# Optimization experiments

Measured on AMD Instinct MI355X. Metric: run time of the kernel, lower is better.

## Reference

```python
import jax, jax.numpy as jnp
import numpy as np

K = 0.001  # sigmoid temperature from DGCLoss init
EPS = 1e-8


def _off_diag(m):
    # [..., n, n] -> [..., n, n-1], removing the diagonal in row-major order
    n = m.shape[-1]
    lead = m.shape[:-2]
    flat = m.reshape(lead + (n * n,))[..., :-1]
    return flat.reshape(lead + (n - 1, n + 1))[..., 1:].reshape(lead + (n, n - 1))


def setup_inputs() -> dict:
    key = jax.random.key(0)
    k1, k2 = jax.random.split(key)
    ranking = jax.random.normal(k1, (384, 256), dtype=jnp.float32)
    gt = jax.random.randint(k2, (384,), 0, 6, dtype=jnp.int64)
    return {"ranking": ranking, "gt": gt}


def reference(ranking, gt):
    x = ranking
    N = x.shape[0]
    # cosine similarity matrix, mapped to [0, 1]
    xn = x / jnp.clip(jnp.linalg.norm(x, axis=1, keepdims=True), EPS, None)
    sm = (xn @ xn.T + 1.0) * 0.5                         # [N, N]
    rank = _off_diag(sm)                                 # [N, N-1]
    g = jnp.abs(gt[None, :] - gt[:, None]).astype(jnp.float32)  # [N, N]
    g = _off_diag(g)                                     # [N, N-1]
    M = N - 1
    # dij[n, i, j] = rank[n, j] - rank[n, i]
    dij = rank[:, None, :] - rank[:, :, None]            # [N, M, M]
    dij = _off_diag(dij)                                 # [N, M, M-1]
    # clamped sigmoid indicator
    indicator = 1.0 / (1.0 + jnp.exp(jnp.clip(-dij / K, -50.0, 50.0)))
    indicator = indicator.sum(-1) + 1.0                  # [N, M]
    relevance = jnp.exp2(jnp.clip(10.0 - g, 0.0, None)) - 1.0  # [N, M]
    dcg = (relevance / jnp.log2(indicator + 1.0)).sum(axis=1)  # [N]
    # ideal DCG from sorted relevance
    rel_sorted = jnp.sort(relevance, axis=-1)[:, ::-1]
    discount = jnp.log2(jnp.arange(M, dtype=jnp.float32) + 2.0)
    idcg = (rel_sorted / discount).sum(axis=-1)          # [N]
    valid = idcg != 0.0
    ndcg = jnp.where(valid, dcg / jnp.where(valid, idcg, 1.0), 0.0)
    cnt = valid.sum()
    mean_ndcg = ndcg.sum() / jnp.maximum(cnt, 1).astype(jnp.float32)
    return jnp.where(cnt == 0, jnp.float32(1.0), 1.0 - mean_ndcg)
```

## Files before the change

kernel.cpp:

```cpp
#include <hip/hip_runtime.h>


#define NN 384
#define DD 256
#define MM 383
#define HSCALE 721.3475204444817f
#define NBUCK  256
#define BSCALE 0.1767955801104972f
#define WWIN   12.0f

__global__ __launch_bounds__(256) void dgc_normT(const float* __restrict__ x,
                                                 float* __restrict__ XT,
                                                 float* __restrict__ XN) {
    __shared__ float xs[16][260];
    __shared__ float invn[16];

    const int t  = threadIdx.x;
    const int r0 = blockIdx.x * 16;

    #pragma unroll
    for (int i = 0; i < 4; ++i) {
        int f = t + i * 256;
        int r = f >> 6, c4 = f & 63;
        float4 v = ((const float4*)(x + (size_t)(r0 + r) * DD))[c4];
        xs[r][c4 * 4 + 0] = v.x; xs[r][c4 * 4 + 1] = v.y;
        xs[r][c4 * 4 + 2] = v.z; xs[r][c4 * 4 + 3] = v.w;
    }
    __syncthreads();

    {
        const int r = t >> 4, sub = t & 15;
        float s = 0.0f;
        #pragma unroll
        for (int m = 0; m < 16; ++m) {
            float v = xs[r][sub * 16 + m];
            s = fmaf(v, v, s);
        }
        #pragma unroll
        for (int off = 8; off > 0; off >>= 1) s += __shfl_xor(s, off, 64);
        if (sub == 0) invn[r] = __builtin_amdgcn_rsqf(fmaxf(s, 1e-16f));
    }
    __syncthreads();

    {
        const int r  = t & 15;
        const int kk = t >> 4;
        const float inv = invn[r];
        #pragma unroll
        for (int i = 0; i < 16; ++i) {
            int k = i * 16 + kk;
            XT[(size_t)k * NN + r0 + r] = xs[r][k] * inv;
        }
    }
    {
        #pragma unroll
        for (int i = 0; i < 4; ++i) {
            int f = t + i * 256;
            int r = f >> 6, c4 = f & 63;
            const float inv = invn[r];
            float4 v;
            v.x = xs[r][c4 * 4 + 0] * inv; v.y = xs[r][c4 * 4 + 1] * inv;
            v.z = xs[r][c4 * 4 + 2] * inv; v.w = xs[r][c4 * 4 + 3] * inv;
            ((float4*)(XN + (size_t)(r0 + r) * DD))[c4] = v;
        }
    }
}

__global__ __launch_bounds__(384) void dgc_fused(const float* __restrict__ XT,
                                                 const float* __restrict__ XN,
                                                 const int* __restrict__ gt,
                                                 float* __restrict__ ndcg) {
    __shared__ float  xs[DD];
    __shared__ float4 pacc[4][96];
    __shared__ float  srow[NN];
    __shared__ float  vsort[NN];
    __shared__ int    sidx[NN];
    __shared__ int    hist[NBUCK];
    __shared__ int    pre[NBUCK + 1];
    __shared__ int    wcnt[6][6];
    __shared__ int    gcum[6];
    __shared__ float  redd[6], redi[6];

    const int n    = blockIdx.x;
    const int t    = threadIdx.x;
    const int lane = t & 63;
    const int wave = t >> 6;

    if (t < DD / 4) ((float4*)xs)[t] = ((const float4*)(XN + (size_t)n * DD))[t];
    if (t < NBUCK) hist[t] = 0;
    __syncthreads();

    {
        const int j4 = t % 96;
        const int kc = t / 96;
        const float4* XT4 = (const float4*)XT;
        float4 a = {0.0f, 0.0f, 0.0f, 0.0f};
        const int k0 = kc * 64;
        #pragma unroll 8
        for (int m = 0; m < 64; ++m) {
            const int k = k0 + m;
            float4 b = XT4[(size_t)k * 96 + j4];
            float  s = xs[k];
            a.x = fmaf(s, b.x, a.x); a.y = fmaf(s, b.y, a.y);
            a.z = fmaf(s, b.z, a.z); a.w = fmaf(s, b.w, a.w);
        }
        pacc[kc][j4] = a;
    }
    __syncthreads();
    {
        const float* pf = (const float*)pacc;
        float dot = pf[t] + pf[384 + t] + pf[768 + t] + pf[1152 + t];
        srow[t] = fmaf(dot, HSCALE, HSCALE);
    }
    __syncthreads();

    const float vraw = srow[t];
    const float sn   = srow[n];

    int b = (int)(vraw * BSCALE);
    b = b < 0 ? 0 : (b > NBUCK - 1 ? NBUCK - 1 : b);
    const int slot = atomicAdd(&hist[b], 1);

    const bool validc = (t < MM);
    int gi = 0;
    if (validc) {
        const int gd = gt[t + (t >= n ? 1 : 0)] - gt[n];
        gi = gd < 0 ? -gd : gd;
    }
    #pragma unroll
    for (int g = 0; g < 6; ++g) {
        unsigned long long m = __ballot(validc && (gi == g));
        if (lane == g) wcnt[wave][g] = __popcll(m);
    }
    __syncthreads();

    if (wave == 0) {
        const int s0 = hist[lane * 4 + 0], s1 = hist[lane * 4 + 1];
        const int s2 = hist[lane * 4 + 2], s3 = hist[lane * 4 + 3];
        const int sum = s0 + s1 + s2 + s3;
        int inc = sum;
        #pragma unroll
        for (int off = 1; off < 64; off <<= 1) {
            int u = __shfl_up(inc, off, 64);
            if (lane >= off) inc += u;
        }
        const int base = inc - sum;
        pre[lane * 4 + 0] = base;
        pre[lane * 4 + 1] = base + s0;
        pre[lane * 4 + 2] = base + s0 + s1;
        pre[lane * 4 + 3] = base + s0 + s1 + s2;
        if (lane == 63) pre[NBUCK] = inc;
    }
    if (t == 0) {
        int s = 0;
        #pragma unroll
        for (int g = 0; g < 6; ++g) {
            s += wcnt[0][g] + wcnt[1][g] + wcnt[2][g]
               + wcnt[3][g] + wcnt[4][g] + wcnt[5][g];
            gcum[g] = s;
        }
    }
    __syncthreads();

    {
        const int pos = pre[b] + slot;
        vsort[pos] = vraw;
        sidx[pos]  = t;
    }
    __syncthreads();

    const float ri    = vsort[t];
    const int   iorig = sidx[t];

    int Blo = (int)((ri - WWIN) * BSCALE);
    int Bhi = (int)((ri + WWIN) * BSCALE);
    Blo = Blo < 0 ? 0 : (Blo > NBUCK - 1 ? NBUCK - 1 : Blo);
    Bhi = Bhi < 0 ? 0 : (Bhi > NBUCK - 1 ? NBUCK - 1 : Bhi);
    const int lo = pre[Blo];
    const int hi = pre[Bhi + 1];

    float p0 = 0.0f, p1 = 0.0f;
    int q = lo;
    for (; q + 2 <= hi; q += 2) {
        p0 += __builtin_amdgcn_rcpf(1.0f + __builtin_amdgcn_exp2f(ri - vsort[q]));
        p1 += __builtin_amdgcn_rcpf(1.0f + __builtin_amdgcn_exp2f(ri - vsort[q + 1]));
    }
    if (q < hi)
        p0 += __builtin_amdgcn_rcpf(1.0f + __builtin_amdgcn_exp2f(ri - vsort[q]));
    float sum_all = (float)(NN - hi) + p0 + p1;

    int bn = (int)(sn * BSCALE);
    bn = bn < 0 ? 0 : (bn > NBUCK - 1 ? NBUCK - 1 : bn);
    float cd = 0.0f;
    if (bn > Bhi)       cd = 1.0f;
    else if (bn >= Blo) cd = __builtin_amdgcn_rcpf(1.0f + __builtin_amdgcn_exp2f(ri - sn));
    const float ind = 0.5f + sum_all - cd;

    float idcg_i = 0.0f;
    if (validc) {
        const int p = t;
        const int g = (p >= gcum[0]) + (p >= gcum[1]) + (p >= gcum[2])
                    + (p >= gcum[3]) + (p >= gcum[4]);
        idcg_i = (float)((1 << (10 - g)) - 1) / __builtin_amdgcn_logf((float)(p + 2));
    }

    float dcg_i = 0.0f;
    if (iorig != n) {
        const int gd = gt[iorig] - gt[n];
        const int gg = gd < 0 ? -gd : gd;
        dcg_i = (float)((1 << (10 - gg)) - 1) / __builtin_amdgcn_logf(ind + 1.0f);
    }

    #pragma unroll
    for (int off = 32; off > 0; off >>= 1) {
        dcg_i  += __shfl_down(dcg_i,  off, 64);
        idcg_i += __shfl_down(idcg_i, off, 64);
    }
    if (lane == 0) { redd[wave] = dcg_i; redi[wave] = idcg_i; }
    __syncthreads();
    if (t == 0) {
        float d = 0.0f, id = 0.0f;
        #pragma unroll
        for (int w = 0; w < 6; ++w) { d += redd[w]; id += redi[w]; }
        ndcg[n] = d / id;
    }
}

__global__ __launch_bounds__(384) void dgc_final(const float* __restrict__ ndcg,
                                                 float* __restrict__ out) {
    __shared__ float red[6];
    const int t    = threadIdx.x;
    const int lane = t & 63;
    const int wave = t >> 6;
    float nd = ndcg[t];
    #pragma unroll
    for (int off = 32; off > 0; off >>= 1) nd += __shfl_down(nd, off, 64);
    if (lane == 0) red[wave] = nd;
    __syncthreads();
    if (t == 0) {
        float s = 0.0f;
        for (int w = 0; w < 6; ++w) s += red[w];
        out[0] = 1.0f - s / (float)NN;
    }
}

extern "C" void kernel_launch(void* const* d_in, const int* in_sizes, int n_in,
                              void* d_out, int out_size, void* d_ws, size_t ws_size,
                              hipStream_t stream) {
    const float* ranking = (const float*)d_in[0];
    const int*   gt      = (const int*)d_in[1];
    float*       out     = (float*)d_out;

    float* XT   = (float*)d_ws;
    float* XN   = XT + (size_t)DD * NN;
    float* ndcg = XN + (size_t)NN * DD;

    dgc_normT<<<24, 256, 0, stream>>>(ranking, XT, XN);
    dgc_fused<<<NN, 384, 0, stream>>>(XT, XN, gt, ndcg);
    dgc_final<<<1, 384, 0, stream>>>(ndcg, out);
}
```

Measured before the change: 73.24 us.

## Process two rows per block, precompute IDCG table, narrow sigmoid window

The fused kernel now handles two query rows per 768-thread block, so each XT column load feeds two dot products and the matrix read traffic is halved. The ideal-DCG sum depends only on the query's gt class, so an extra block in the normalisation kernel computes it once into a six-entry table, which removes per-row ballot counting and a reduction. The sigmoid evaluation window shrinks from 12 to 6 scaled units, so fewer pairs are evaluated exactly. The narrower window adds approximation error for pairs whose sigmoid is not yet saturated, and the larger blocks use more shared memory, which may reduce occupancy.

After: 70.10 us. 1.04x faster.

```diff
diff --git a/kernel.cpp b/kernel.cpp
--- a/kernel.cpp
+++ b/kernel.cpp
@@ -7,15 +7,69 @@
 #define HSCALE 721.3475204444817f
 #define NBUCK  256
 #define BSCALE 0.1767955801104972f
-#define WWIN   12.0f
+#define WWIN   6.0f
 
 __global__ __launch_bounds__(256) void dgc_normT(const float* __restrict__ x,
+                                                 const int* __restrict__ gt,
                                                  float* __restrict__ XT,
-                                                 float* __restrict__ XN) {
+                                                 float* __restrict__ XN,
+                                                 float* __restrict__ idcg_tab) {
+    const int t = threadIdx.x;
+
+    if (blockIdx.x == 24) {
+        __shared__ int   cnt[6];
+        __shared__ int   cum[6][6];
+        __shared__ float wred[4][6];
+        const int lane = t & 63;
+        const int wave = t >> 6;
+
+        if (t < 6) cnt[t] = 0;
+        __syncthreads();
+        atomicAdd(&cnt[gt[t]], 1);
+        if (t + 256 < NN) atomicAdd(&cnt[gt[t + 256]], 1);
+        __syncthreads();
+        if (t < 6) {
+            int h[6];
+            #pragma unroll
+            for (int g = 0; g < 6; ++g) h[g] = 0;
+            #pragma unroll
+            for (int v = 0; v < 6; ++v) {
+                int d = v - t; d = d < 0 ? -d : d;
+                h[d] += cnt[v];
+            }
+            h[0] -= 1;
+            int s = 0;
+            #pragma unroll
+            for (int g = 0; g < 6; ++g) { s += h[g]; cum[t][g] = s; }
+        }
+        __syncthreads();
+
+        float acc[6] = {0.f, 0.f, 0.f, 0.f, 0.f, 0.f};
+        for (int p = t; p < MM; p += 256) {
+            const float invl = 1.0f / __builtin_amdgcn_logf((float)(p + 2));
+            #pragma unroll
+            for (int gv = 0; gv < 6; ++gv) {
+                const int g = (p >= cum[gv][0]) + (p >= cum[gv][1])
+                            + (p >= cum[gv][2]) + (p >= cum[gv][3])
+                            + (p >= cum[gv][4]);
+                acc[gv] += (float)((1 << (10 - g)) - 1) * invl;
+            }
+        }
+        for (int off = 32; off > 0; off >>= 1) {
+            #pragma unroll
+            for (int gv = 0; gv < 6; ++gv) acc[gv] += __shfl_down(acc[gv], off, 64);
+        }
+        if (lane == 0) {
+            #pragma unroll
+            for (int gv = 0; gv < 6; ++gv) wred[wave][gv] = acc[gv];
+        }
+        __syncthreads();
+        if (t < 6) idcg_tab[t] = wred[0][t] + wred[1][t] + wred[2][t] + wred[3][t];
+        return;
+    }
+
     __shared__ float xs[16][260];
     __shared__ float invn[16];
-
-    const int t  = threadIdx.x;
     const int r0 = blockIdx.x * 16;
 
     #pragma unroll
@@ -66,127 +120,119 @@
     }
 }
 
-__global__ __launch_bounds__(384) void dgc_fused(const float* __restrict__ XT,
+__global__ __launch_bounds__(768) void dgc_fused(const float* __restrict__ XT,
                                                  const float* __restrict__ XN,
                                                  const int* __restrict__ gt,
+                                                 const float* __restrict__ idcg_tab,
                                                  float* __restrict__ ndcg) {
-    __shared__ float  xs[DD];
-    __shared__ float4 pacc[4][96];
-    __shared__ float  srow[NN];
-    __shared__ float  vsort[NN];
-    __shared__ int    sidx[NN];
-    __shared__ int    hist[NBUCK];
-    __shared__ int    pre[NBUCK + 1];
-    __shared__ int    wcnt[6][6];
-    __shared__ int    gcum[6];
-    __shared__ float  redd[6], redi[6];
-
-    const int n    = blockIdx.x;
+    __shared__ float  xs[2][DD];
+    __shared__ float4 pacc[2][8][96];
+    __shared__ float  srow[2][NN];
+    __shared__ float  vsort[2][NN];
+    __shared__ int    sidx[2][NN];
+    __shared__ int    hist[2][NBUCK];
+    __shared__ int    pre[2][NBUCK + 1];
+    __shared__ float  redd[12];
+
+    const int n0   = blockIdx.x * 2;
     const int t    = threadIdx.x;
     const int lane = t & 63;
     const int wave = t >> 6;
 
-    if (t < DD / 4) ((float4*)xs)[t] = ((const float4*)(XN + (size_t)n * DD))[t];
-    if (t < NBUCK) hist[t] = 0;
+    if (t < 128)
+        ((float4*)xs[t >> 6])[t & 63] =
+            ((const float4*)(XN + (size_t)(n0 + (t >> 6)) * DD))[t & 63];
+    if (t < 512) ((int*)hist)[t] = 0;
     __syncthreads();
 
     {
         const int j4 = t % 96;
         const int kc = t / 96;
         const float4* XT4 = (const float4*)XT;
-        float4 a = {0.0f, 0.0f, 0.0f, 0.0f};
-        const int k0 = kc * 64;
+        float4 a0 = {0.f, 0.f, 0.f, 0.f};
+        float4 a1 = {0.f, 0.f, 0.f, 0.f};
+        const int k0 = kc * 32;
         #pragma unroll 8
-        for (int m = 0; m < 64; ++m) {
+        for (int m = 0; m < 32; ++m) {
             const int k = k0 + m;
             float4 b = XT4[(size_t)k * 96 + j4];
-            float  s = xs[k];
-            a.x = fmaf(s, b.x, a.x); a.y = fmaf(s, b.y, a.y);
-            a.z = fmaf(s, b.z, a.z); a.w = fmaf(s, b.w, a.w);
-        }
-        pacc[kc][j4] = a;
-    }
-    __syncthreads();
-    {
-        const float* pf = (const float*)pacc;
-        float dot = pf[t] + pf[384 + t] + pf[768 + t] + pf[1152 + t];
-        srow[t] = fmaf(dot, HSCALE, HSCALE);
-    }
-    __syncthreads();
-
-    const float vraw = srow[t];
-    const float sn   = srow[n];
-
+            float s0 = xs[0][k];
+            float s1 = xs[1][k];
+            a0.x = fmaf(s0, b.x, a0.x); a0.y = fmaf(s0, b.y, a0.y);
+            a0.z = fmaf(s0, b.z, a0.z); a0.w = fmaf(s0, b.w, a0.w);
+            a1.x = fmaf(s1, b.x, a1.x); a1.y = fmaf(s1, b.y, a1.y);
+            a1.z = fmaf(s1, b.z, a1.z); a1.w = fmaf(s1, b.w, a1.w);
+        }
+        pacc[0][kc][j4] = a0;
+        pacc[1][kc][j4] = a1;
+    }
+    __syncthreads();
+
+    const int r = t / 384;
+    const int u = t - r * 384;
+
+    {
+        const float* pf = (const float*)pacc[r];
+        float dot = 0.0f;
+        #pragma unroll
+        for (int c = 0; c < 8; ++c) dot += pf[c * 384 + u];
+        srow[r][u] = fmaf(dot, HSCALE, HSCALE);
+    }
+    __syncthreads();
+
+    const float vraw = srow[r][u];
     int b = (int)(vraw * BSCALE);
     b = b < 0 ? 0 : (b > NBUCK - 1 ? NBUCK - 1 : b);
-    const int slot = atomicAdd(&hist[b], 1);
-
-    const bool validc = (t < MM);
-    int gi = 0;
-    if (validc) {
-        const int gd = gt[t + (t >= n ? 1 : 0)] - gt[n];
-        gi = gd < 0 ? -gd : gd;
-    }
-    #pragma unroll
-    for (int g = 0; g < 6; ++g) {
-        unsigned long long m = __ballot(validc && (gi == g));
-        if (lane == g) wcnt[wave][g] = __popcll(m);
-    }
-    __syncthreads();
-
-    if (wave == 0) {
-        const int s0 = hist[lane * 4 + 0], s1 = hist[lane * 4 + 1];
-        const int s2 = hist[lane * 4 + 2], s3 = hist[lane * 4 + 3];
+    const int slot = atomicAdd(&hist[r][b], 1);
+    __syncthreads();
+
+    if (wave == 0 || wave == 6) {
+        const int rr = wave / 6;
+        const int s0 = hist[rr][lane * 4 + 0], s1 = hist[rr][lane * 4 + 1];
+        const int s2 = hist[rr][lane * 4 + 2], s3 = hist[rr][lane * 4 + 3];
         const int sum = s0 + s1 + s2 + s3;
         int inc = sum;
         #pragma unroll
         for (int off = 1; off < 64; off <<= 1) {
-            int u = __shfl_up(inc, off, 64);
-            if (lane >= off) inc += u;
+            int uu = __shfl_up(inc, off, 64);
+            if (lane >= off) inc += uu;
         }
         const int base = inc - sum;
-        pre[lane * 4 + 0] = base;
-        pre[lane * 4 + 1] = base + s0;
-        pre[lane * 4 + 2] = base + s0 + s1;
-        pre[lane * 4 + 3] = base + s0 + s1 + s2;
-        if (lane == 63) pre[NBUCK] = inc;
-    }
-    if (t == 0) {
-        int s = 0;
-        #pragma unroll
-        for (int g = 0; g < 6; ++g) {
-            s += wcnt[0][g] + wcnt[1][g] + wcnt[2][g]
-               + wcnt[3][g] + wcnt[4][g] + wcnt[5][g];
-            gcum[g] = s;
-        }
-    }
-    __syncthreads();
-
-    {
-        const int pos = pre[b] + slot;
-        vsort[pos] = vraw;
-        sidx[pos]  = t;
-    }
-    __syncthreads();
-
-    const float ri    = vsort[t];
-    const int   iorig = sidx[t];
+        pre[rr][lane * 4 + 0] = base;
+        pre[rr][lane * 4 + 1] = base + s0;
+        pre[rr][lane * 4 + 2] = base + s0 + s1;
+        pre[rr][lane * 4 + 3] = base + s0 + s1 + s2;
+        if (lane == 63) pre[rr][NBUCK] = inc;
+    }
+    __syncthreads();
+
+    {
+        const int pos = pre[r][b] + slot;
+        vsort[r][pos] = vraw;
+        sidx[r][pos]  = u;
+    }
+    __syncthreads();
+
+    const int   nrow  = n0 + r;
+    const float ri    = vsort[r][u];
+    const int   iorig = sidx[r][u];
+    const float sn    = srow[r][nrow];
 
     int Blo = (int)((ri - WWIN) * BSCALE);
     int Bhi = (int)((ri + WWIN) * BSCALE);
     Blo = Blo < 0 ? 0 : (Blo > NBUCK - 1 ? NBUCK - 1 : Blo);
     Bhi = Bhi < 0 ? 0 : (Bhi > NBUCK - 1 ? NBUCK - 1 : Bhi);
-    const int lo = pre[Blo];
-    const int hi = pre[Bhi + 1];
+    const int lo = pre[r][Blo];
+    const int hi = pre[r][Bhi + 1];
 
     float p0 = 0.0f, p1 = 0.0f;
     int q = lo;
     for (; q + 2 <= hi; q += 2) {
-        p0 += __builtin_amdgcn_rcpf(1.0f + __builtin_amdgcn_exp2f(ri - vsort[q]));
-        p1 += __builtin_amdgcn_rcpf(1.0f + __builtin_amdgcn_exp2f(ri - vsort[q + 1]));
+        p0 += __builtin_amdgcn_rcpf(1.0f + __builtin_amdgcn_exp2f(ri - vsort[r][q]));
+        p1 += __builtin_amdgcn_rcpf(1.0f + __builtin_amdgcn_exp2f(ri - vsort[r][q + 1]));
     }
     if (q < hi)
-        p0 += __builtin_amdgcn_rcpf(1.0f + __builtin_amdgcn_exp2f(ri - vsort[q]));
+        p0 += __builtin_amdgcn_rcpf(1.0f + __builtin_amdgcn_exp2f(ri - vsort[r][q]));
     float sum_all = (float)(NN - hi) + p0 + p1;
 
     int bn = (int)(sn * BSCALE);
@@ -196,34 +242,23 @@
     else if (bn >= Blo) cd = __builtin_amdgcn_rcpf(1.0f + __builtin_amdgcn_exp2f(ri - sn));
     const float ind = 0.5f + sum_all - cd;
 
-    float idcg_i = 0.0f;
-    if (validc) {
-        const int p = t;
-        const int g = (p >= gcum[0]) + (p >= gcum[1]) + (p >= gcum[2])
-                    + (p >= gcum[3]) + (p >= gcum[4]);
-        idcg_i = (float)((1 << (10 - g)) - 1) / __builtin_amdgcn_logf((float)(p + 2));
-    }
-
     float dcg_i = 0.0f;
-    if (iorig != n) {
-        const int gd = gt[iorig] - gt[n];
+    if (iorig != nrow) {
+        const int gd = gt[iorig] - gt[nrow];
         const int gg = gd < 0 ? -gd : gd;
         dcg_i = (float)((1 << (10 - gg)) - 1) / __builtin_amdgcn_logf(ind + 1.0f);
     }
 
     #pragma unroll
-    for (int off = 32; off > 0; off >>= 1) {
-        dcg_i  += __shfl_down(dcg_i,  off, 64);
-        idcg_i += __shfl_down(idcg_i, off, 64);
-    }
-    if (lane == 0) { redd[wave] = dcg_i; redi[wave] = idcg_i; }
-    __syncthreads();
-    if (t == 0) {
-        float d = 0.0f, id = 0.0f;
-        #pragma unroll
-        for (int w = 0; w < 6; ++w) { d += redd[w]; id += redi[w]; }
-        ndcg[n] = d / id;
-    }
+    for (int off = 32; off > 0; off >>= 1) dcg_i += __shfl_down(dcg_i, off, 64);
+    if (lane == 0) redd[wave] = dcg_i;
+    __syncthreads();
+    if (t == 0)
+        ndcg[n0] = (redd[0] + redd[1] + redd[2] + redd[3] + redd[4] + redd[5])
+                   / idcg_tab[gt[n0]];
+    if (t == 384)
+        ndcg[n0 + 1] = (redd[6] + redd[7] + redd[8] + redd[9] + redd[10] + redd[11])
+                       / idcg_tab[gt[n0 + 1]];
 }
 
 __global__ __launch_bounds__(384) void dgc_final(const float* __restrict__ ndcg,
@@ -254,8 +289,9 @@
     float* XT   = (float*)d_ws;
     float* XN   = XT + (size_t)DD * NN;
     float* ndcg = XN + (size_t)NN * DD;
-
-    dgc_normT<<<24, 256, 0, stream>>>(ranking, XT, XN);
-    dgc_fused<<<NN, 384, 0, stream>>>(XT, XN, gt, ndcg);
+    float* tab  = ndcg + NN;
+
+    dgc_normT<<<25, 256, 0, stream>>>(ranking, gt, XT, XN, tab);
+    dgc_fused<<<NN / 2, 768, 0, stream>>>(XT, XN, gt, tab, ndcg);
     dgc_final<<<1, 384, 0, stream>>>(ndcg, out);
 }
```
